# Performance work log

Hardware: AMD Instinct MI355X
Metric: run time of the kernel (lower is better)

## Reference

```python
import jax, jax.numpy as jnp
import numpy as np

B, K, PS, DP = 8, 8, 128, 16           # batch, patches/example, patch px, dino patch size
D, NH, HD, L = 1024, 8, 128, 2         # embed dim, heads, head dim, transformer layers
GRID = PS // DP                        # 8 tokens per side
TPP = GRID * GRID                      # 64 tokens per patch


def _conv(x, w, stride, pad):
    return jax.lax.conv_general_dilated(x, w, (stride, stride), pad,
                                        dimension_numbers=('NCHW', 'OIHW', 'NCHW'))


def _ln(x, g, b, eps=1e-5):
    m = jnp.mean(x, -1, keepdims=True)
    v = jnp.var(x, -1, keepdims=True)
    return (x - m) * jax.lax.rsqrt(v + eps) * g + b


def _bn(x, g, b, m, v, eps=1e-5):
    inv = jax.lax.rsqrt(v + eps)
    return (x - m[:, None, None]) * inv[:, None, None] * g[:, None, None] + b[:, None, None]


def _up2(x):  # bilinear x2, align_corners=False (half-pixel, matches jax.image.resize)
    n, c, h, w = x.shape
    return jax.image.resize(x, (n, c, 2 * h, 2 * w), method='linear')


def _mha(x, wqkv, bqkv, wo, bo):
    b, s, d = x.shape
    qkv = x @ wqkv.T + bqkv
    q, k, v = jnp.split(qkv, 3, axis=-1)
    q = q.reshape(b, s, NH, HD).transpose(0, 2, 1, 3)
    k = k.reshape(b, s, NH, HD).transpose(0, 2, 1, 3)
    v = v.reshape(b, s, NH, HD).transpose(0, 2, 1, 3)
    att = jax.nn.softmax(jnp.einsum('bhqd,bhkd->bhqk', q, k) / jnp.sqrt(jnp.float32(HD)), axis=-1)
    o = jnp.einsum('bhqk,bhkd->bhqd', att, v).transpose(0, 2, 1, 3).reshape(b, s, d)
    return o @ wo.T + bo


def setup_inputs() -> dict:
    key = jax.random.key(0)
    ks = iter(jax.random.split(key, 40))

    def rn(shape, s=0.02):
        return jax.random.normal(next(ks), shape, jnp.float32) * s

    inp = {}
    inp['patches'] = jax.random.normal(next(ks), (B, K, 3, PS, PS), jnp.float32)
    inp['pe_w'] = rn((D, 3, DP, DP))
    inp['pe_b'] = jnp.zeros((D,), jnp.float32)
    inp['qkv_w'] = rn((L, 3 * D, D))
    inp['qkv_b'] = jnp.zeros((L, 3 * D), jnp.float32)
    inp['out_w'] = rn((L, D, D))
    inp['out_b'] = jnp.zeros((L, D), jnp.float32)
    inp['ln1_g'] = jnp.ones((L, D), jnp.float32)
    inp['ln1_b'] = jnp.zeros((L, D), jnp.float32)
    inp['ff1_w'] = rn((L, 4 * D, D))
    inp['ff1_b'] = jnp.zeros((L, 4 * D), jnp.float32)
    inp['ff2_w'] = rn((L, D, 4 * D))
    inp['ff2_b'] = jnp.zeros((L, D), jnp.float32)
    inp['ln2_g'] = jnp.ones((L, D), jnp.float32)
    inp['ln2_b'] = jnp.zeros((L, D), jnp.float32)
    chans = [(512, D), (256, 512), (128, 256), (64, 128)]
    for i, (co, ci) in enumerate(chans, 1):
        inp[f'dw{i}'] = rn((co, ci, 3, 3), 0.05)
        inp[f'db{i}'] = jnp.zeros((co,), jnp.float32)
        inp[f'g{i}'] = jnp.ones((co,), jnp.float32)
        inp[f'be{i}'] = jnp.zeros((co,), jnp.float32)
        inp[f'm{i}'] = jnp.zeros((co,), jnp.float32)
        inp[f'v{i}'] = jnp.ones((co,), jnp.float32)
    inp['dw5'] = rn((1, 64, 1, 1), 0.05)
    inp['db5'] = jnp.zeros((1,), jnp.float32)
    return inp


def reference(patches, pe_w, pe_b, qkv_w, qkv_b, out_w, out_b, ln1_g, ln1_b,
              ff1_w, ff1_b, ff2_w, ff2_b, ln2_g, ln2_b,
              dw1, db1, g1, be1, m1, v1, dw2, db2, g2, be2, m2, v2,
              dw3, db3, g3, be3, m3, v3, dw4, db4, g4, be4, m4, v4, dw5, db5):
    b, k = patches.shape[:2]
    x = patches.reshape(b * k, 3, PS, PS)
    # frozen DINO patch embedding (runs under torch.no_grad in the original)
    hs = _conv(x, pe_w, DP, 'VALID') + pe_b[None, :, None, None]     # [BK, D, GRID, GRID]
    hs = jax.lax.stop_gradient(hs)
    hs = hs.reshape(b * k, D, TPP).transpose(0, 2, 1).reshape(b, k * TPP, D)
    # post-norm TransformerEncoder (norm_first=False, gelu), dropout=eval (identity)
    for i in range(L):
        hs = _ln(hs + _mha(hs, qkv_w[i], qkv_b[i], out_w[i], out_b[i]), ln1_g[i], ln1_b[i])
        ff = jax.nn.gelu(hs @ ff1_w[i].T + ff1_b[i], approximate=False) @ ff2_w[i].T + ff2_b[i]
        hs = _ln(hs + ff, ln2_g[i], ln2_b[i])
    fm = hs.reshape(b * k, TPP, D).transpose(0, 2, 1).reshape(b * k, D, GRID, GRID)
    # CNN decoder: (conv3x3 -> BN(eval) -> ReLU -> bilinear x2) x4 -> conv1x1
    y = _up2(jax.nn.relu(_bn(_conv(fm, dw1, 1, 'SAME') + db1[None, :, None, None], g1, be1, m1, v1)))
    y = _up2(jax.nn.relu(_bn(_conv(y, dw2, 1, 'SAME') + db2[None, :, None, None], g2, be2, m2, v2)))
    y = _up2(jax.nn.relu(_bn(_conv(y, dw3, 1, 'SAME') + db3[None, :, None, None], g3, be3, m3, v3)))
    y = _up2(jax.nn.relu(_bn(_conv(y, dw4, 1, 'SAME') + db4[None, :, None, None], g4, be4, m4, v4)))
    y = _conv(y, dw5, 1, 'VALID') + db5[None, :, None, None]          # [BK, 1, PS, PS]
    return y.reshape(b, k, 1, PS, PS)
```

## Files before the change

### kernel.cpp

```cpp
#include <hip/hip_runtime.h>
#include <stdint.h>


typedef unsigned short u16;
typedef __bf16 bf16x8 __attribute__((ext_vector_type(8)));
typedef short  s16x8  __attribute__((ext_vector_type(8)));
typedef float  f32x4  __attribute__((ext_vector_type(4)));

__device__ __forceinline__ float b2f(u16 x) { return __uint_as_float(((unsigned)x) << 16); }
__device__ __forceinline__ u16 f2b(float f) {
  unsigned u = __float_as_uint(f);
  unsigned r = (u + 0x7fffu + ((u >> 16) & 1u)) >> 16;
  return (u16)r;
}
__device__ __forceinline__ void async16(u16* lds, const u16* g) {
  __builtin_amdgcn_global_load_lds((const __attribute__((address_space(1))) void*)g,
                                   (__attribute__((address_space(3))) void*)lds, 16, 0, 0);
}
__device__ __forceinline__ float gelu_f(float x) {
  return 0.5f * x * (1.0f + erff(x * 0.70710678118654752f));
}

__global__ __launch_bounds__(256) void cvt_f2b(const float* __restrict__ src,
                                               u16* __restrict__ dst, int n) {
  const int i = (blockIdx.x * 256 + threadIdx.x) * 4;
  if (i + 3 < n) {
    const float4 v = *(const float4*)(src + i);
    dst[i] = f2b(v.x); dst[i + 1] = f2b(v.y); dst[i + 2] = f2b(v.z); dst[i + 3] = f2b(v.w);
  }
}

__global__ __launch_bounds__(256) void gemm_bt(
    const u16* __restrict__ A, int lda, long long sAb, long long sAh,
    const u16* __restrict__ B, int ldb, long long sBb, long long sBh,
    u16* __restrict__ Cb, int ldc, long long sCb, long long sCh,
    const float* __restrict__ bias, int epi, int ZH, int nk,
    float* __restrict__ Part)
{
  __shared__ u16 As[3][128 * 32];
  __shared__ u16 Bs[3][128 * 32];
  const int tid = threadIdx.x;
  const int zb = blockIdx.z / ZH, zh = blockIdx.z % ZH;
  const u16* Ab = A + zb * sAb + zh * sAh;
  const u16* Bb = B + zb * sBb + zh * sBh;
  const int m0 = blockIdx.y << 7, n0 = blockIdx.x << 7;
  const int wave = tid >> 6, lane = tid & 63;
  const int wm = (wave >> 1) << 6, wn = (wave & 1) << 6;
  const int lr = lane & 15, lq = lane >> 4;
  const int rowb = tid >> 2;
  const int koff = Part ? (zb * (nk << 5)) : 0;
  const int kc_e = (((tid & 3) ^ ((tid >> 3) & 3)) << 3);
  const int kslot = ((lq ^ ((lr >> 1) & 3)) << 3);

  const u16* Arow0 = Ab + (long long)(m0 + rowb)      * lda + kc_e + koff;
  const u16* Arow1 = Ab + (long long)(m0 + rowb + 64) * lda + kc_e + koff;
  const u16* Brow0 = Bb + (long long)(n0 + rowb)      * ldb + kc_e + koff;
  const u16* Brow1 = Bb + (long long)(n0 + rowb + 64) * ldb + kc_e + koff;

  f32x4 acc[4][4] = {};

  auto stage = [&](int kt, int b) {
    const int k0 = kt << 5;
    async16(&As[b][tid * 8],         Arow0 + k0);
    async16(&As[b][(tid + 256) * 8], Arow1 + k0);
    async16(&Bs[b][tid * 8],         Brow0 + k0);
    async16(&Bs[b][(tid + 256) * 8], Brow1 + k0);
  };

  stage(0, 0);
  if (nk > 1) stage(1, 1);
  int cur = 0;
  for (int kt = 0; kt < nk; ++kt) {
    if (kt + 2 < nk) {
      int nb = cur + 2; if (nb >= 3) nb -= 3;
      stage(kt + 2, nb);
      asm volatile("s_waitcnt vmcnt(8)" ::: "memory");
    } else if (kt + 1 < nk) {
      asm volatile("s_waitcnt vmcnt(4)" ::: "memory");
    } else {
      asm volatile("s_waitcnt vmcnt(0)" ::: "memory");
    }
    asm volatile("s_barrier" ::: "memory");

    bf16x8 af[4], bfv[4];
#pragma unroll
    for (int mi = 0; mi < 4; ++mi)
      af[mi] = __builtin_bit_cast(bf16x8, *(const s16x8*)&As[cur][((wm + mi * 16 + lr) << 5) + kslot]);
#pragma unroll
    for (int ni = 0; ni < 4; ++ni)
      bfv[ni] = __builtin_bit_cast(bf16x8, *(const s16x8*)&Bs[cur][((wn + ni * 16 + lr) << 5) + kslot]);
#pragma unroll
    for (int mi = 0; mi < 4; ++mi)
#pragma unroll
      for (int ni = 0; ni < 4; ++ni)
        acc[mi][ni] = __builtin_amdgcn_mfma_f32_16x16x32_bf16(af[mi], bfv[ni], acc[mi][ni], 0, 0, 0);

    asm volatile("s_barrier" ::: "memory");
    ++cur; if (cur == 3) cur = 0;
  }

  if (Part) {
    float* P = Part + (long long)zb * sCb;
#pragma unroll
    for (int ni = 0; ni < 4; ++ni) {
      const int col = n0 + wn + ni * 16 + lr;
#pragma unroll
      for (int mi = 0; mi < 4; ++mi) {
        const int row0 = m0 + wm + mi * 16 + (lq << 2);
#pragma unroll
        for (int r = 0; r < 4; ++r)
          P[(long long)(row0 + r) * ldc + col] = acc[mi][ni][r];
      }
    }
    return;
  }

  const long long Co = zb * sCb + zh * sCh;
#pragma unroll
  for (int ni = 0; ni < 4; ++ni) {
    const int col = n0 + wn + ni * 16 + lr;
    const float badd = bias ? bias[col] : 0.0f;
#pragma unroll
    for (int mi = 0; mi < 4; ++mi) {
      const int row0 = m0 + wm + mi * 16 + (lq << 2);
#pragma unroll
      for (int r = 0; r < 4; ++r) {
        float v = acc[mi][ni][r] + badd;
        if (epi == 1) v = gelu_f(v);
        Cb[Co + (long long)(row0 + r) * ldc + col] = f2b(v);
      }
    }
  }
}

__global__ __launch_bounds__(256) void reduce_bias(
    const float* __restrict__ Part, long long sPart, int S,
    const float* __restrict__ bias, int N,
    u16* __restrict__ Out, long long total)
{
  const long long i = ((long long)blockIdx.x * 256 + threadIdx.x) * 4;
  if (i >= total) return;
  f32x4 s = *(const f32x4*)(Part + i);
  for (int p = 1; p < S; ++p) {
    const f32x4 v = *(const f32x4*)(Part + (long long)p * sPart + i);
    s[0] += v[0]; s[1] += v[1]; s[2] += v[2]; s[3] += v[3];
  }
  const int colb = (int)(i & (N - 1));
#pragma unroll
  for (int j = 0; j < 4; ++j)
    Out[i + j] = f2b(s[j] + bias[colb + j]);
}

__global__ __launch_bounds__(256) void reduce_bn(
    const float* __restrict__ Part, long long sPart, int S,
    const float* __restrict__ bn_g, const float* __restrict__ bn_b,
    const float* __restrict__ bn_m, const float* __restrict__ bn_v,
    const float* __restrict__ cb, int Cout,
    u16* __restrict__ Out, long long total)
{
  const long long i = ((long long)blockIdx.x * 256 + threadIdx.x) * 4;
  if (i >= total) return;
  f32x4 s = *(const f32x4*)(Part + i);
  for (int p = 1; p < S; ++p) {
    const f32x4 v = *(const f32x4*)(Part + (long long)p * sPart + i);
    s[0] += v[0]; s[1] += v[1]; s[2] += v[2]; s[3] += v[3];
  }
  const int colb = (int)(i & (Cout - 1));
#pragma unroll
  for (int j = 0; j < 4; ++j) {
    const int col = colb + j;
    const float inv = rsqrtf(bn_v[col] + 1e-5f);
    const float bs = bn_g[col] * inv;
    const float bsh = (cb[col] - bn_m[col]) * bs + bn_b[col];
    Out[i + j] = f2b(fmaxf(s[j] * bs + bsh, 0.0f));
  }
}

__global__ __launch_bounds__(256) void conv_gemm(
    const u16* __restrict__ U, const u16* __restrict__ Wr,
    u16* __restrict__ Out,
    const float* __restrict__ bn_g, const float* __restrict__ bn_b,
    const float* __restrict__ bn_m, const float* __restrict__ bn_v,
    const float* __restrict__ cb,
    const u16* __restrict__ zpg,
    int H, int W, int l2w, int l2hw, int l2c, int CoutReal, int Kdim, int nk,
    float* __restrict__ Part, long long sPart)
{
  __shared__ u16 As[3][128 * 32];
  __shared__ u16 Bs[3][64 * 32];
  const int tid = threadIdx.x;
  const int m0 = blockIdx.x << 7, n0 = blockIdx.y << 6;
  const int slice = blockIdx.z;
  const int koff = Part ? (slice * (nk << 5)) : 0;
  const int wave = tid >> 6, lane = tid & 63;
  const int wm = (wave >> 1) << 6, wn = (wave & 1) << 5;
  const int lr = lane & 15, lq = lane >> 4;
  const int rowb = tid >> 2;
  const int kc_e = (((tid & 3) ^ ((tid >> 3) & 3)) << 3);
  const int kslot = ((lq ^ ((lr >> 1) & 3)) << 3);
  const int hwmask = (1 << l2hw) - 1, wmask = (1 << l2w) - 1, cmask = (1 << l2c) - 1;

  int yA[2], xA[2];
  long long baseA[2];
  {
#pragma unroll
    for (int i = 0; i < 2; ++i) {
      const int mrow = m0 + rowb + (i << 6);
      const int img = mrow >> l2hw;
      const int rem = mrow & hwmask;
      yA[i] = rem >> l2w; xA[i] = rem & wmask;
      baseA[i] = (long long)(img << l2hw);
    }
  }
  const u16* Bbase = Wr + (long long)(n0 + rowb) * Kdim + kc_e + koff;

  f32x4 acc[4][2] = {};

  auto stage = [&](int kt, int b) {
    const int k0 = kt << 5;
    const int kabs = koff + k0 + kc_e;
    const int t = kabs >> l2c, ci = kabs & cmask;
    const int dy = (t * 86) >> 8;
    const int dx = t - dy * 3;
#pragma unroll
    for (int i = 0; i < 2; ++i) {
      const int yy = yA[i] + dy - 1, xx = xA[i] + dx - 1;
      const u16* src = ((unsigned)yy < (unsigned)H && (unsigned)xx < (unsigned)W)
          ? U + (((baseA[i] + (yy << l2w) + xx) << l2c) + ci)
          : zpg;
      async16(&As[b][(tid + (i << 8)) * 8], src);
    }
    async16(&Bs[b][tid * 8], Bbase + k0);
  };

  stage(0, 0);
  stage(1, 1);

  for (int t0 = 0; t0 < nk; t0 += 3) {
#pragma unroll
    for (int p = 0; p < 3; ++p) {
      const int tt = t0 + p;
      if (tt + 2 < nk) {
        stage(tt + 2, (p + 2) % 3);
        asm volatile("s_waitcnt vmcnt(6)" ::: "memory");
      } else if (tt + 1 < nk) {
        asm volatile("s_waitcnt vmcnt(3)" ::: "memory");
      } else {
        asm volatile("s_waitcnt vmcnt(0)" ::: "memory");
      }
      asm volatile("s_barrier" ::: "memory");

      bf16x8 af[4], bfv[2];
#pragma unroll
      for (int mi = 0; mi < 4; ++mi)
        af[mi] = __builtin_bit_cast(bf16x8, *(const s16x8*)&As[p][((wm + mi * 16 + lr) << 5) + kslot]);
#pragma unroll
      for (int ni = 0; ni < 2; ++ni)
        bfv[ni] = __builtin_bit_cast(bf16x8, *(const s16x8*)&Bs[p][((wn + ni * 16 + lr) << 5) + kslot]);
#pragma unroll
      for (int mi = 0; mi < 4; ++mi)
#pragma unroll
        for (int ni = 0; ni < 2; ++ni)
          acc[mi][ni] = __builtin_amdgcn_mfma_f32_16x16x32_bf16(af[mi], bfv[ni], acc[mi][ni], 0, 0, 0);

      asm volatile("s_barrier" ::: "memory");
    }
  }

  if (Part) {
    float* P = Part + (long long)slice * sPart;
#pragma unroll
    for (int ni = 0; ni < 2; ++ni) {
      const int col = n0 + wn + ni * 16 + lr;
#pragma unroll
      for (int mi = 0; mi < 4; ++mi) {
        const int row0 = m0 + wm + mi * 16 + (lq << 2);
#pragma unroll
        for (int r = 0; r < 4; ++r)
          P[(long long)(row0 + r) * CoutReal + col] = acc[mi][ni][r];
      }
    }
    return;
  }

#pragma unroll
  for (int ni = 0; ni < 2; ++ni) {
    const int col = n0 + wn + ni * 16 + lr;
    const bool ok = col < CoutReal;
    float bs = 0.0f, bsh = 0.0f;
    if (ok) {
      const float inv = rsqrtf(bn_v[col] + 1e-5f);
      bs = bn_g[col] * inv;
      bsh = (cb[col] - bn_m[col]) * bs + bn_b[col];
    }
#pragma unroll
    for (int mi = 0; mi < 4; ++mi) {
      const int row0 = m0 + wm + mi * 16 + (lq << 2);
#pragma unroll
      for (int r = 0; r < 4; ++r) {
        if (ok) {
          const float v = fmaxf(acc[mi][ni][r] * bs + bsh, 0.0f);
          Out[(long long)(row0 + r) * CoutReal + col] = f2b(v);
        }
      }
    }
  }
}


__global__ void pe_gather(const float* __restrict__ patches, u16* __restrict__ Ape) {
  const int t = blockIdx.x, tid = threadIdx.x;
  const int img = t >> 6, pos = t & 63, ty = pos >> 3, tx = pos & 7;
  const float* base = patches + (long long)img * 3 * 128 * 128;
  u16* dst = Ape + (long long)t * 768;
  for (int k = tid; k < 768; k += 256) {
    const int c = k >> 8, rr = k & 255, ky = rr >> 4, kx = rr & 15;
    dst[k] = f2b(base[c * 16384 + (ty * 16 + ky) * 128 + tx * 16 + kx]);
  }
}

__global__ void vt_transpose(const u16* __restrict__ qkv, u16* __restrict__ Vt) {
  __shared__ u16 lds[64 * 130];
  const int tt = blockIdx.x;
  const int z = blockIdx.y;
  const int bq = z >> 3, h = z & 7;
  const int tid = threadIdx.x;
  for (int idx = tid; idx < 64 * 128; idx += 256) {
    const int t = idx >> 7, d = idx & 127;
    lds[t * 130 + d] = qkv[(long long)(bq * 512 + tt * 64 + t) * 3072 + 2048 + h * 128 + d];
  }
  __syncthreads();
  for (int idx = tid; idx < 64 * 128; idx += 256) {
    const int d = idx >> 6, t = idx & 63;
    Vt[(long long)z * 65536 + d * 512 + tt * 64 + t] = lds[t * 130 + d];
  }
}

__global__ __launch_bounds__(256) void softmax_rows(u16* __restrict__ P) {
  __shared__ float red[8];
  const long long base = (long long)blockIdx.x * 512;
  const int tid = threadIdx.x;
  const float sc = 0.08838834764831845f;
  float x0 = b2f(P[base + tid]) * sc;
  float x1 = b2f(P[base + tid + 256]) * sc;
  float mx = fmaxf(x0, x1);
  for (int o = 32; o; o >>= 1) mx = fmaxf(mx, __shfl_down(mx, o));
  if ((tid & 63) == 0) red[tid >> 6] = mx;
  __syncthreads();
  mx = fmaxf(fmaxf(red[0], red[1]), fmaxf(red[2], red[3]));
  const float e0 = expf(x0 - mx), e1 = expf(x1 - mx);
  float s = e0 + e1;
  for (int o = 32; o; o >>= 1) s += __shfl_down(s, o);
  __syncthreads();
  if ((tid & 63) == 0) red[tid >> 6] = s;
  __syncthreads();
  s = red[0] + red[1] + red[2] + red[3];
  const float inv = 1.0f / s;
  P[base + tid] = f2b(e0 * inv);
  P[base + tid + 256] = f2b(e1 * inv);
}

__global__ __launch_bounds__(256) void ln_kernel(
    u16* __restrict__ hsb, const u16* __restrict__ P,
    const float* __restrict__ gw, const float* __restrict__ bw)
{
  __shared__ float red[8];
  const int r = blockIdx.x, tid = threadIdx.x;
  float x[4], s = 0.0f, s2 = 0.0f;
#pragma unroll
  for (int i = 0; i < 4; ++i) {
    const int c = tid + i * 256;
    const float v = b2f(hsb[(long long)r * 1024 + c]) + b2f(P[(long long)r * 1024 + c]);
    x[i] = v; s += v; s2 += v * v;
  }
  for (int o = 32; o; o >>= 1) { s += __shfl_down(s, o); s2 += __shfl_down(s2, o); }
  if ((tid & 63) == 0) { red[tid >> 6] = s; red[4 + (tid >> 6)] = s2; }
  __syncthreads();
  s  = red[0] + red[1] + red[2] + red[3];
  s2 = red[4] + red[5] + red[6] + red[7];
  const float mean = s * (1.0f / 1024.0f);
  const float var = s2 * (1.0f / 1024.0f) - mean * mean;
  const float inv = rsqrtf(var + 1e-5f);
#pragma unroll
  for (int i = 0; i < 4; ++i) {
    const int c = tid + i * 256;
    const float y = (x[i] - mean) * inv * gw[c] + bw[c];
    hsb[(long long)r * 1024 + c] = f2b(y);
  }
}

__global__ void repack_w(const float* __restrict__ src, u16* __restrict__ dst, int Cout, int l2c) {
  const int co = blockIdx.x, tid = threadIdx.x;
  const int Cin = 1 << l2c, K9 = 9 << l2c;
  for (int j = tid; j < K9; j += 256) {
    const int t = j >> l2c, ci = j & (Cin - 1);
    u16 v = 0;
    if (co < Cout) v = f2b(src[(long long)(co * Cin + ci) * 9 + t]);
    dst[(long long)co * K9 + j] = v;
  }
}

__global__ void ups2x(const u16* __restrict__ in, u16* __restrict__ out,
                      int l2h, int l2w, int l2c, long long total)
{
  const long long idx = (long long)blockIdx.x * 256 + threadIdx.x;
  if (idx >= total) return;
  const int H = 1 << l2h, W = 1 << l2w, C = 1 << l2c;
  const int c = (int)(idx & (C - 1));
  long long t = idx >> l2c;
  const int ox = (int)(t & (2 * W - 1)); t >>= (l2w + 1);
  const int oy = (int)(t & (2 * H - 1)); t >>= (l2h + 1);
  const int img = (int)t;
  const int iy = oy >> 1, ix = ox >> 1;
  int y0, y1, x0, x1; float wy0, wy1, wx0, wx1;
  if (oy & 1) { y0 = iy; y1 = min(iy + 1, H - 1); wy0 = 0.75f; wy1 = 0.25f; }
  else        { y0 = max(iy - 1, 0); y1 = iy;     wy0 = 0.25f; wy1 = 0.75f; }
  if (ox & 1) { x0 = ix; x1 = min(ix + 1, W - 1); wx0 = 0.75f; wx1 = 0.25f; }
  else        { x0 = max(ix - 1, 0); x1 = ix;     wx0 = 0.25f; wx1 = 0.75f; }
  const u16* base = in + (((long long)img) << (l2h + l2w + l2c));
  const float v00 = b2f(base[((((long long)y0 << l2w) + x0) << l2c) + c]);
  const float v01 = b2f(base[((((long long)y0 << l2w) + x1) << l2c) + c]);
  const float v10 = b2f(base[((((long long)y1 << l2w) + x0) << l2c) + c]);
  const float v11 = b2f(base[((((long long)y1 << l2w) + x1) << l2c) + c]);
  out[idx] = f2b(wy0 * (wx0 * v00 + wx1 * v01) + wy1 * (wx0 * v10 + wx1 * v11));
}

__global__ __launch_bounds__(256) void conv1x1_final(
    const u16* __restrict__ C4, const float* __restrict__ w5,
    const float* __restrict__ b5, float* __restrict__ Z)
{
  const int tid = threadIdx.x;
  const int px = blockIdx.x * 4 + (tid >> 6);
  const int lane = tid & 63;
  float v = b2f(C4[(long long)px * 64 + lane]) * w5[lane];
  for (int o = 32; o; o >>= 1) v += __shfl_down(v, o);
  if (lane == 0) Z[px] = v + b5[0];
}

__global__ void ups_final(const float* __restrict__ Z, float* __restrict__ out) {
  const int idx = blockIdx.x * 256 + threadIdx.x;
  const int ox = idx & 127, oy = (idx >> 7) & 127, img = idx >> 14;
  const int iy = oy >> 1, ix = ox >> 1;
  int y0, y1, x0, x1; float wy0, wy1, wx0, wx1;
  if (oy & 1) { y0 = iy; y1 = min(iy + 1, 63); wy0 = 0.75f; wy1 = 0.25f; }
  else        { y0 = max(iy - 1, 0); y1 = iy;  wy0 = 0.25f; wy1 = 0.75f; }
  if (ox & 1) { x0 = ix; x1 = min(ix + 1, 63); wx0 = 0.75f; wx1 = 0.25f; }
  else        { x0 = max(ix - 1, 0); x1 = ix;  wx0 = 0.25f; wx1 = 0.75f; }
  const float* zi = Z + (long long)img * 4096;
  const float v = wy0 * (wx0 * zi[y0 * 64 + x0] + wx1 * zi[y0 * 64 + x1]) +
                  wy1 * (wx0 * zi[y1 * 64 + x0] + wx1 * zi[y1 * 64 + x1]);
  out[idx] = v;
}

extern "C" void kernel_launch(void* const* d_in, const int* in_sizes, int n_in,
                              void* d_out, int out_size, void* d_ws, size_t ws_size,
                              hipStream_t stream)
{
  (void)in_sizes; (void)n_in; (void)out_size;
  if (ws_size < 110395648u) return;
  const float* patches = (const float*)d_in[0];
  const float* pe_w = (const float*)d_in[1];
  const float* pe_b = (const float*)d_in[2];
  const float* qkv_w = (const float*)d_in[3];
  const float* qkv_b = (const float*)d_in[4];
  const float* out_w = (const float*)d_in[5];
  const float* out_b = (const float*)d_in[6];
  const float* ln1_g = (const float*)d_in[7];
  const float* ln1_b = (const float*)d_in[8];
  const float* ff1_w = (const float*)d_in[9];
  const float* ff1_b = (const float*)d_in[10];
  const float* ff2_w = (const float*)d_in[11];
  const float* ff2_b = (const float*)d_in[12];
  const float* ln2_g = (const float*)d_in[13];
  const float* ln2_b = (const float*)d_in[14];
  const float* dwv[4] = {(const float*)d_in[15], (const float*)d_in[21], (const float*)d_in[27], (const float*)d_in[33]};
  const float* dbv[4] = {(const float*)d_in[16], (const float*)d_in[22], (const float*)d_in[28], (const float*)d_in[34]};
  const float* gv[4]  = {(const float*)d_in[17], (const float*)d_in[23], (const float*)d_in[29], (const float*)d_in[35]};
  const float* bev[4] = {(const float*)d_in[18], (const float*)d_in[24], (const float*)d_in[30], (const float*)d_in[36]};
  const float* mv[4]  = {(const float*)d_in[19], (const float*)d_in[25], (const float*)d_in[31], (const float*)d_in[37]};
  const float* vv[4]  = {(const float*)d_in[20], (const float*)d_in[26], (const float*)d_in[32], (const float*)d_in[38]};
  const float* dw5 = (const float*)d_in[39];
  const float* db5 = (const float*)d_in[40];
  float* outp = (float*)d_out;
  char* ws = (char*)d_ws;

  u16* HS_B = (u16*)(ws + 0);
  u16* APE  = (u16*)(ws + 8388608);
  u16* QKV  = (u16*)(ws + 8388608);
  u16* VT   = (u16*)(ws + 33554432);
  u16* SF   = (u16*)(ws + 41943040);
  u16* FF1G = (u16*)(ws + 41943040);
  u16* ATT  = (u16*)(ws + 75497472);
  u16* P_B  = (u16*)(ws + 83886080);
  u16* W1   = (u16*)(ws + 92274688);
  u16* W2   = (u16*)(ws + 100663296);
  float* PART_G  = (float*)(ws + 8388608);
  float* PART_PE = (float*)(ws + 41943040);
  u16* WR1 = (u16*)(ws + 8388608);
  u16* WR2 = (u16*)(ws + 17825792);
  u16* WR3 = (u16*)(ws + 20185088);
  u16* C1  = (u16*)(ws + 20774912);
  u16* U1  = (u16*)(ws + 24969216);
  u16* C2  = (u16*)(ws + 41746432);
  u16* U2  = (u16*)(ws + 50135040);
  u16* C3  = (u16*)(ws + 83689472);
  u16* U3  = (u16*)(ws + 8388608);
  u16* C4  = (u16*)(ws + 75497472);
  float* PARTC1 = (float*)(ws + 41746432);
  float* PARTC2 = (float*)(ws + 50331648);
  u16* ZPG = (u16*)(ws + 109051904);
  u16* WR4 = (u16*)(ws + 109052160);
  float* Z = (float*)(ws + 109347072);

  pe_gather<<<4096, 256, 0, stream>>>(patches, APE);
  cvt_f2b<<<768, 256, 0, stream>>>(pe_w, W1, 786432);
  gemm_bt<<<dim3(8, 32, 2), 256, 0, stream>>>(
      APE, 768, 0, 0, W1, 768, 0, 0,
      HS_B, 1024, 4194304, 0, nullptr, 0, 1, 12, PART_PE);
  reduce_bias<<<4096, 256, 0, stream>>>(PART_PE, 4194304, 2, pe_b, 1024, HS_B, 4194304LL);

  for (int l = 0; l < 2; ++l) {
    cvt_f2b<<<3072, 256, 0, stream>>>(qkv_w + (long long)l * 3145728, W1, 3145728);
    gemm_bt<<<dim3(24, 32, 1), 256, 0, stream>>>(
        HS_B, 1024, 0, 0, W1, 1024, 0, 0,
        QKV, 3072, 0, 0, qkv_b + l * 3072, 0, 1, 32, nullptr);
    vt_transpose<<<dim3(8, 64), 256, 0, stream>>>(QKV, VT);
    gemm_bt<<<dim3(4, 4, 64), 256, 0, stream>>>(
        QKV, 3072, 1572864, 128, QKV + 1024, 3072, 1572864, 128,
        SF, 512, 2097152, 262144, nullptr, 0, 8, 4, nullptr);
    softmax_rows<<<32768, 256, 0, stream>>>(SF);
    gemm_bt<<<dim3(1, 4, 64), 256, 0, stream>>>(
        SF, 512, 2097152, 262144, VT, 512, 524288, 65536,
        ATT, 1024, 524288, 128, nullptr, 0, 8, 16, nullptr);
    cvt_f2b<<<1024, 256, 0, stream>>>(out_w + (long long)l * 1048576, W2, 1048576);
    gemm_bt<<<dim3(8, 32, 2), 256, 0, stream>>>(
        ATT, 1024, 0, 0, W2, 1024, 0, 0,
        P_B, 1024, 4194304, 0, nullptr, 0, 1, 16, PART_G);
    reduce_bias<<<4096, 256, 0, stream>>>(PART_G, 4194304, 2, out_b + l * 1024, 1024, P_B, 4194304LL);
    ln_kernel<<<4096, 256, 0, stream>>>(HS_B, P_B, ln1_g + l * 1024, ln1_b + l * 1024);
    cvt_f2b<<<4096, 256, 0, stream>>>(ff1_w + (long long)l * 4194304, W1, 4194304);
    cvt_f2b<<<4096, 256, 0, stream>>>(ff2_w + (long long)l * 4194304, W2, 4194304);
    gemm_bt<<<dim3(32, 32, 1), 256, 0, stream>>>(
        HS_B, 1024, 0, 0, W1, 1024, 0, 0,
        FF1G, 4096, 0, 0, ff1_b + l * 4096, 1, 1, 32, nullptr);
    gemm_bt<<<dim3(8, 32, 2), 256, 0, stream>>>(
        FF1G, 4096, 0, 0, W2, 4096, 0, 0,
        P_B, 1024, 4194304, 0, nullptr, 0, 1, 64, PART_G);
    reduce_bias<<<4096, 256, 0, stream>>>(PART_G, 4194304, 2, ff2_b + l * 1024, 1024, P_B, 4194304LL);
    ln_kernel<<<4096, 256, 0, stream>>>(HS_B, P_B, ln2_g + l * 1024, ln2_b + l * 1024);
  }

  hipMemsetAsync((void*)ZPG, 0, 256, stream);
  repack_w<<<512, 256, 0, stream>>>(dwv[0], WR1, 512, 10);
  repack_w<<<256, 256, 0, stream>>>(dwv[1], WR2, 256, 9);
  repack_w<<<128, 256, 0, stream>>>(dwv[2], WR3, 128, 8);
  repack_w<<<128, 256, 0, stream>>>(dwv[3], WR4, 64, 7);

  conv_gemm<<<dim3(32, 8, 4), 256, 0, stream>>>(
      HS_B, WR1, C1, gv[0], bev[0], mv[0], vv[0], dbv[0], ZPG,
      8, 8, 3, 6, 10, 512, 9216, 72, PARTC1, 2097152);
  reduce_bn<<<2048, 256, 0, stream>>>(PARTC1, 2097152, 4,
      gv[0], bev[0], mv[0], vv[0], dbv[0], 512, C1, 2097152LL);
  ups2x<<<32768, 256, 0, stream>>>(C1, U1, 3, 3, 9, 8388608LL);
  conv_gemm<<<dim3(128, 4, 2), 256, 0, stream>>>(
      U1, WR2, C2, gv[1], bev[1], mv[1], vv[1], dbv[1], ZPG,
      16, 16, 4, 8, 9, 256, 4608, 72, PARTC2, 4194304);
  reduce_bn<<<4096, 256, 0, stream>>>(PARTC2, 4194304, 2,
      gv[1], bev[1], mv[1], vv[1], dbv[1], 256, C2, 4194304LL);
  ups2x<<<65536, 256, 0, stream>>>(C2, U2, 4, 4, 8, 16777216LL);
  conv_gemm<<<dim3(512, 2, 1), 256, 0, stream>>>(
      U2, WR3, C3, gv[2], bev[2], mv[2], vv[2], dbv[2], ZPG,
      32, 32, 5, 10, 8, 128, 2304, 72, nullptr, 0);
  ups2x<<<131072, 256, 0, stream>>>(C3, U3, 5, 5, 7, 33554432LL);
  conv_gemm<<<dim3(2048, 1, 1), 256, 0, stream>>>(
      U3, WR4, C4, gv[3], bev[3], mv[3], vv[3], dbv[3], ZPG,
      64, 64, 6, 12, 7, 64, 1152, 36, nullptr, 0);
  conv1x1_final<<<65536, 256, 0, stream>>>(C4, dw5, db5, Z);
  ups_final<<<4096, 256, 0, stream>>>(Z, outp);
}
```

Measured before the change: 1.306 ms.

## Template conv_gemm and precompute per-tap source pointers with channel-block-major K order

The implicit-GEMM convolution is templated on width, channel count and K-tile count, so index math becomes compile-time. The loop now iterates channel blocks outer and the 9 taps inner, with all 18 tap source pointers precomputed per thread, which removes per-stage division and bounds checks. The split-K partition now splits over channel blocks rather than contiguous K. This means the reordered weight offsets and the zero page, enlarged to cover channel offsets, must stay consistent. Workspace offsets for WR4 and Z are moved to fit the larger zero page, which costs extra registers for the pointer table.

```diff
diff --git a/kernel.cpp b/kernel.cpp
--- a/kernel.cpp
+++ b/kernel.cpp
@@ -176,6 +176,7 @@
   }
 }
 
+template <int L2W, int L2C, int NK>
 __global__ __launch_bounds__(256) void conv_gemm(
     const u16* __restrict__ U, const u16* __restrict__ Wr,
     u16* __restrict__ Out,
@@ -183,89 +184,101 @@
     const float* __restrict__ bn_m, const float* __restrict__ bn_v,
     const float* __restrict__ cb,
     const u16* __restrict__ zpg,
-    int H, int W, int l2w, int l2hw, int l2c, int CoutReal, int Kdim, int nk,
+    int CoutReal,
     float* __restrict__ Part, long long sPart)
 {
+  constexpr int L2HW = 2 * L2W;
+  constexpr int HH = 1 << L2W;
+  constexpr int Kdim = 9 << L2C;
+  constexpr int OD = NK / 9;
   __shared__ u16 As[3][128 * 32];
   __shared__ u16 Bs[3][64 * 32];
   const int tid = threadIdx.x;
   const int m0 = blockIdx.x << 7, n0 = blockIdx.y << 6;
   const int slice = blockIdx.z;
-  const int koff = Part ? (slice * (nk << 5)) : 0;
+  const int gdbase = slice * OD;
   const int wave = tid >> 6, lane = tid & 63;
   const int wm = (wave >> 1) << 6, wn = (wave & 1) << 5;
   const int lr = lane & 15, lq = lane >> 4;
   const int rowb = tid >> 2;
   const int kc_e = (((tid & 3) ^ ((tid >> 3) & 3)) << 3);
   const int kslot = ((lq ^ ((lr >> 1) & 3)) << 3);
-  const int hwmask = (1 << l2hw) - 1, wmask = (1 << l2w) - 1, cmask = (1 << l2c) - 1;
-
-  int yA[2], xA[2];
-  long long baseA[2];
-  {
-#pragma unroll
-    for (int i = 0; i < 2; ++i) {
-      const int mrow = m0 + rowb + (i << 6);
-      const int img = mrow >> l2hw;
-      const int rem = mrow & hwmask;
-      yA[i] = rem >> l2w; xA[i] = rem & wmask;
-      baseA[i] = (long long)(img << l2hw);
-    }
-  }
-  const u16* Bbase = Wr + (long long)(n0 + rowb) * Kdim + kc_e + koff;
+  const int ciStart = (gdbase << 5) + kc_e;
+
+  const u16* Pt[2][9];
+#pragma unroll
+  for (int i = 0; i < 2; ++i) {
+    const int mrow = m0 + rowb + (i << 6);
+    const int img = mrow >> L2HW;
+    const int rem = mrow & ((1 << L2HW) - 1);
+    const int y = rem >> L2W, x = rem & (HH - 1);
+    const long long ibase = (long long)img << L2HW;
+#pragma unroll
+    for (int tap = 0; tap < 9; ++tap) {
+      const int dy = tap / 3, dx = tap % 3;
+      const int yy = y + dy - 1, xx = x + dx - 1;
+      Pt[i][tap] = ((unsigned)yy < (unsigned)HH && (unsigned)xx < (unsigned)HH)
+          ? U + ((((ibase + (yy << L2W) + xx)) << L2C) + ciStart)
+          : zpg + ciStart;
+    }
+  }
+  const u16* Bp = Wr + (long long)(n0 + rowb) * Kdim + kc_e + (gdbase << 5);
 
   f32x4 acc[4][2] = {};
 
-  auto stage = [&](int kt, int b) {
-    const int k0 = kt << 5;
-    const int kabs = koff + k0 + kc_e;
-    const int t = kabs >> l2c, ci = kabs & cmask;
-    const int dy = (t * 86) >> 8;
-    const int dx = t - dy * 3;
-#pragma unroll
-    for (int i = 0; i < 2; ++i) {
-      const int yy = yA[i] + dy - 1, xx = xA[i] + dx - 1;
-      const u16* src = ((unsigned)yy < (unsigned)H && (unsigned)xx < (unsigned)W)
-          ? U + (((baseA[i] + (yy << l2w) + xx) << l2c) + ci)
-          : zpg;
-      async16(&As[b][(tid + (i << 8)) * 8], src);
-    }
-    async16(&Bs[b][tid * 8], Bbase + k0);
-  };
-
-  stage(0, 0);
-  stage(1, 1);
-
-  for (int t0 = 0; t0 < nk; t0 += 3) {
-#pragma unroll
-    for (int p = 0; p < 3; ++p) {
-      const int tt = t0 + p;
-      if (tt + 2 < nk) {
-        stage(tt + 2, (p + 2) % 3);
-        asm volatile("s_waitcnt vmcnt(6)" ::: "memory");
-      } else if (tt + 1 < nk) {
-        asm volatile("s_waitcnt vmcnt(3)" ::: "memory");
-      } else {
-        asm volatile("s_waitcnt vmcnt(0)" ::: "memory");
-      }
+#define STAGE(TAP, CIE, B)                                                 \
+  do {                                                                    \
+    async16(&As[(B)][tid * 8],         Pt[0][(TAP)] + (CIE));             \
+    async16(&As[(B)][(tid + 256) * 8], Pt[1][(TAP)] + (CIE));             \
+    async16(&Bs[(B)][tid * 8],         Bp + (CIE) + ((TAP) << L2C));      \
+  } while (0)
+
+#define COMPUTE(B)                                                         \
+  do {                                                                    \
+    bf16x8 af[4], bfv[2];                                                 \
+    _Pragma("unroll") for (int mi = 0; mi < 4; ++mi)                      \
+      af[mi] = __builtin_bit_cast(bf16x8,                                 \
+        *(const s16x8*)&As[(B)][((wm + mi * 16 + lr) << 5) + kslot]);     \
+    _Pragma("unroll") for (int ni = 0; ni < 2; ++ni)                      \
+      bfv[ni] = __builtin_bit_cast(bf16x8,                                \
+        *(const s16x8*)&Bs[(B)][((wn + ni * 16 + lr) << 5) + kslot]);     \
+    _Pragma("unroll") for (int mi = 0; mi < 4; ++mi)                      \
+      _Pragma("unroll") for (int ni = 0; ni < 2; ++ni)                    \
+        acc[mi][ni] = __builtin_amdgcn_mfma_f32_16x16x32_bf16(            \
+            af[mi], bfv[ni], acc[mi][ni], 0, 0, 0);                       \
+  } while (0)
+
+  STAGE(0, 0, 0);
+  STAGE(1, 0, 1);
+
+  int ciOff = 0;
+  for (int od = 0; od < OD - 1; ++od, ciOff += 32) {
+#pragma unroll
+    for (int tap = 0; tap < 9; ++tap) {
+      if (tap < 7) STAGE(tap + 2, ciOff, (tap + 2) % 3);
+      else         STAGE(tap - 7, ciOff + 32, (tap + 2) % 3);
+      asm volatile("s_waitcnt vmcnt(6)" ::: "memory");
       asm volatile("s_barrier" ::: "memory");
-
-      bf16x8 af[4], bfv[2];
-#pragma unroll
-      for (int mi = 0; mi < 4; ++mi)
-        af[mi] = __builtin_bit_cast(bf16x8, *(const s16x8*)&As[p][((wm + mi * 16 + lr) << 5) + kslot]);
-#pragma unroll
-      for (int ni = 0; ni < 2; ++ni)
-        bfv[ni] = __builtin_bit_cast(bf16x8, *(const s16x8*)&Bs[p][((wn + ni * 16 + lr) << 5) + kslot]);
-#pragma unroll
-      for (int mi = 0; mi < 4; ++mi)
-#pragma unroll
-        for (int ni = 0; ni < 2; ++ni)
-          acc[mi][ni] = __builtin_amdgcn_mfma_f32_16x16x32_bf16(af[mi], bfv[ni], acc[mi][ni], 0, 0, 0);
-
+      COMPUTE(tap % 3);
       asm volatile("s_barrier" ::: "memory");
     }
   }
+#pragma unroll
+  for (int tap = 0; tap < 9; ++tap) {
+    if (tap < 7) {
+      STAGE(tap + 2, ciOff, (tap + 2) % 3);
+      asm volatile("s_waitcnt vmcnt(6)" ::: "memory");
+    } else if (tap == 7) {
+      asm volatile("s_waitcnt vmcnt(3)" ::: "memory");
+    } else {
+      asm volatile("s_waitcnt vmcnt(0)" ::: "memory");
+    }
+    asm volatile("s_barrier" ::: "memory");
+    COMPUTE(tap % 3);
+    asm volatile("s_barrier" ::: "memory");
+  }
+#undef STAGE
+#undef COMPUTE
 
   if (Part) {
     float* P = Part + (long long)slice * sPart;
@@ -509,8 +522,8 @@
   float* PARTC1 = (float*)(ws + 41746432);
   float* PARTC2 = (float*)(ws + 50331648);
   u16* ZPG = (u16*)(ws + 109051904);
-  u16* WR4 = (u16*)(ws + 109052160);
-  float* Z = (float*)(ws + 109347072);
+  u16* WR4 = (u16*)(ws + 109056000);
+  float* Z = (float*)(ws + 8388608);
 
   pe_gather<<<4096, 256, 0, stream>>>(patches, APE);
   cvt_f2b<<<768, 256, 0, stream>>>(pe_w, W1, 786432);
@@ -550,31 +563,31 @@
     ln_kernel<<<4096, 256, 0, stream>>>(HS_B, P_B, ln2_g + l * 1024, ln2_b + l * 1024);
   }
 
-  hipMemsetAsync((void*)ZPG, 0, 256, stream);
+  hipMemsetAsync((void*)ZPG, 0, 4096, stream);
   repack_w<<<512, 256, 0, stream>>>(dwv[0], WR1, 512, 10);
   repack_w<<<256, 256, 0, stream>>>(dwv[1], WR2, 256, 9);
   repack_w<<<128, 256, 0, stream>>>(dwv[2], WR3, 128, 8);
   repack_w<<<128, 256, 0, stream>>>(dwv[3], WR4, 64, 7);
 
-  conv_gemm<<<dim3(32, 8, 4), 256, 0, stream>>>(
+  conv_gemm<3, 10, 72><<<dim3(32, 8, 4), 256, 0, stream>>>(
       HS_B, WR1, C1, gv[0], bev[0], mv[0], vv[0], dbv[0], ZPG,
-      8, 8, 3, 6, 10, 512, 9216, 72, PARTC1, 2097152);
+      512, PARTC1, 2097152);
   reduce_bn<<<2048, 256, 0, stream>>>(PARTC1, 2097152, 4,
       gv[0], bev[0], mv[0], vv[0], dbv[0], 512, C1, 2097152LL);
   ups2x<<<32768, 256, 0, stream>>>(C1, U1, 3, 3, 9, 8388608LL);
-  conv_gemm<<<dim3(128, 4, 2), 256, 0, stream>>>(
+  conv_gemm<4, 9, 72><<<dim3(128, 4, 2), 256, 0, stream>>>(
       U1, WR2, C2, gv[1], bev[1], mv[1], vv[1], dbv[1], ZPG,
-      16, 16, 4, 8, 9, 256, 4608, 72, PARTC2, 4194304);
+      256, PARTC2, 4194304);
   reduce_bn<<<4096, 256, 0, stream>>>(PARTC2, 4194304, 2,
       gv[1], bev[1], mv[1], vv[1], dbv[1], 256, C2, 4194304LL);
   ups2x<<<65536, 256, 0, stream>>>(C2, U2, 4, 4, 8, 16777216LL);
-  conv_gemm<<<dim3(512, 2, 1), 256, 0, stream>>>(
+  conv_gemm<5, 8, 72><<<dim3(512, 2, 1), 256, 0, stream>>>(
       U2, WR3, C3, gv[2], bev[2], mv[2], vv[2], dbv[2], ZPG,
-      32, 32, 5, 10, 8, 128, 2304, 72, nullptr, 0);
+      128, nullptr, 0);
   ups2x<<<131072, 256, 0, stream>>>(C3, U3, 5, 5, 7, 33554432LL);
-  conv_gemm<<<dim3(2048, 1, 1), 256, 0, stream>>>(
+  conv_gemm<6, 7, 36><<<dim3(2048, 1, 1), 256, 0, stream>>>(
       U3, WR4, C4, gv[3], bev[3], mv[3], vv[3], dbv[3], ZPG,
-      64, 64, 6, 12, 7, 64, 1152, 36, nullptr, 0);
+      64, nullptr, 0);
   conv1x1_final<<<65536, 256, 0, stream>>>(C4, dw5, db5, Z);
   ups_final<<<4096, 256, 0, stream>>>(Z, outp);
 }
```

Result: no change. 1.299 ms (-0.5%).
